# Performance work log

Measured on AMD Instinct MI355X. Metric: run time of the kernel, lower is better.

The kernel has to match this reference:

```python
import jax, jax.numpy as jnp
import numpy as np

B, T, C, H = 2, 2048, 2048, 16
HD = C // H  # 128 head dim
ROPE_BASE = 10000.0


def setup_inputs() -> dict:
    key = jax.random.key(0)
    k0, k1, k2 = jax.random.split(key, 3)
    x = jax.random.normal(k0, (B, T, C), dtype=jnp.float32)
    W_attn = jax.random.normal(k1, (C, 3 * C), dtype=jnp.float32) * 0.02
    b_attn = jnp.zeros((3 * C,), dtype=jnp.float32)
    W_proj = jax.random.normal(k2, (C, C), dtype=jnp.float32) * 0.02
    b_proj = jnp.zeros((C,), dtype=jnp.float32)
    # freqs_cis = exp(i * t * theta_j), represented as (cos, sin), shape [T, HD//2]
    inv_freq = 1.0 / (ROPE_BASE ** (jnp.arange(0, HD, 2, dtype=jnp.float32) / HD))
    freqs = jnp.outer(jnp.arange(T, dtype=jnp.float32), inv_freq)
    return {"x": x, "W_attn": W_attn, "b_attn": b_attn, "W_proj": W_proj,
            "b_proj": b_proj, "cos": jnp.cos(freqs), "sin": jnp.sin(freqs)}


def _apply_rope(v, cos, sin):
    # v: [B, T, H, HD]; pairs (v[..., 2i], v[..., 2i+1]) rotated by angle freqs[t, i]
    vr = v.reshape(v.shape[:-1] + (-1, 2))
    x0, x1 = vr[..., 0], vr[..., 1]
    c = cos[None, :, None, :]  # [1, T, 1, HD//2]
    s = sin[None, :, None, :]
    o0 = x0 * c - x1 * s
    o1 = x0 * s + x1 * c
    return jnp.stack([o0, o1], axis=-1).reshape(v.shape)


def reference(x, W_attn, b_attn, W_proj, b_proj, cos, sin):
    Bv, Tv, Cv = x.shape
    qkv = x @ W_attn + b_attn                      # [B, T, 3C]
    q, k, v = jnp.split(qkv, 3, axis=-1)
    q = q.reshape(Bv, Tv, H, HD)
    k = k.reshape(Bv, Tv, H, HD)
    v = v.reshape(Bv, Tv, H, HD)
    q = _apply_rope(q, cos, sin)
    k = _apply_rope(k, cos, sin)
    scale = 1.0 / jnp.sqrt(jnp.float32(HD))
    att = jnp.einsum('bqhd,bkhd->bhqk', q, k) * scale
    causal = jnp.tril(jnp.ones((Tv, Tv), dtype=bool))
    att = jnp.where(causal[None, None], att, jnp.finfo(att.dtype).min)
    att = jax.nn.softmax(att, axis=-1)
    y = jnp.einsum('bhqk,bkhd->bqhd', att, v).reshape(Bv, Tv, Cv)
    return y @ W_proj + b_proj
```

## Files before the change

### kernel.cpp

```cpp
#include <hip/hip_runtime.h>

typedef unsigned short u16;
typedef __attribute__((ext_vector_type(8))) short short8;
typedef __attribute__((ext_vector_type(4))) float f32x4;

#define TSEQ 2048
#define NHEAD 16
#define HDIM 128

__device__ __forceinline__ u16 f2bf(float x) {
    unsigned u = __float_as_uint(x);
    return (u16)((u + 0x7fffu + ((u >> 16) & 1u)) >> 16);
}
__device__ __forceinline__ float b2f(u16 h) {
    return __uint_as_float(((unsigned)h) << 16);
}
__device__ __forceinline__ void async16(const void* g, void* l) {
    __builtin_amdgcn_global_load_lds((__attribute__((address_space(1))) void*)(void*)g,
                                     (__attribute__((address_space(3))) void*)l, 16, 0, 0);
}
__device__ __forceinline__ f32x4 zero4() {
    f32x4 z = {0.f, 0.f, 0.f, 0.f};
    return z;
}

template <int CTRL>
__device__ __forceinline__ float dppf(float x) {
    return __int_as_float(__builtin_amdgcn_mov_dpp(__float_as_int(x), CTRL, 0xf, 0xf, true));
}
__device__ __forceinline__ float dpp_max16(float x) {
    x = fmaxf(x, dppf<0xB1>(x));
    x = fmaxf(x, dppf<0x4E>(x));
    x = fmaxf(x, dppf<0x141>(x));
    x = fmaxf(x, dppf<0x140>(x));
    return x;
}
__device__ __forceinline__ float dpp_sum16(float x) {
    x += dppf<0xB1>(x);
    x += dppf<0x4E>(x);
    x += dppf<0x141>(x);
    x += dppf<0x140>(x);
    return x;
}

__global__ void cast_bf16(const float4* __restrict__ in, ushort4* __restrict__ out, int n4) {
    int i = blockIdx.x * 256 + threadIdx.x;
    if (i < n4) {
        float4 v = in[i];
        ushort4 o;
        o.x = f2bf(v.x); o.y = f2bf(v.y); o.z = f2bf(v.z); o.w = f2bf(v.w);
        out[i] = o;
    }
}

__global__ void transpose_cast(const float* __restrict__ in, u16* __restrict__ out, int K, int N) {
    __shared__ float tile[64][65];
    int n0 = blockIdx.x * 64, k0 = blockIdx.y * 64;
    int tx = threadIdx.x & 63, ty = threadIdx.x >> 6;
#pragma unroll
    for (int i = 0; i < 16; i++) {
        int r = ty + i * 4;
        tile[r][tx] = in[(size_t)(k0 + r) * N + n0 + tx];
    }
    __syncthreads();
#pragma unroll
    for (int i = 0; i < 16; i++) {
        int r = ty + i * 4;
        out[(size_t)(n0 + r) * K + k0 + tx] = f2bf(tile[tx][r]);
    }
}

template <int MODE>
__global__ __launch_bounds__(256) void gemm_bt(
    const u16* __restrict__ A, const u16* __restrict__ Bt, const float* __restrict__ bias,
    float* __restrict__ outf, u16* __restrict__ qb, u16* __restrict__ kb, u16* __restrict__ vT,
    const float* __restrict__ cosp, const float* __restrict__ sinp,
    int M, int N, int K) {
    __shared__ __align__(16) u16 smem[8704];
    u16* As = smem;
    u16* Bs = smem + 4096;
    const int tid = threadIdx.x;
    const int wave = tid >> 6, lane = tid & 63;
    const int low = lane & 15, quad = lane >> 4;
    const int m0 = blockIdx.y * 128, n0 = blockIdx.x * 128;
    const int wm = (wave >> 1) * 64, wn = (wave & 1) * 64;
    const int ldr = lane >> 2;
    const int ldc = (lane & 3) * 8;

    f32x4 acc[4][4];
#pragma unroll
    for (int i = 0; i < 4; i++)
#pragma unroll
        for (int j = 0; j < 4; j++) acc[i][j] = zero4();

    for (int k0 = 0; k0 < K; k0 += 32) {
#pragma unroll
        for (int c = 0; c < 2; ++c) {
            const int chunk = wave * 2 + c;
            const int row = chunk * 16 + ldr;
            async16(A + (size_t)(m0 + row) * K + k0 + ldc, As + chunk * 512);
            async16(Bt + (size_t)(n0 + row) * K + k0 + ldc, Bs + chunk * 512);
        }
        __syncthreads();
        short8 af[4], bfv[4];
#pragma unroll
        for (int i = 0; i < 4; i++) af[i] = *(const short8*)(As + (wm + i * 16 + low) * 32 + quad * 8);
#pragma unroll
        for (int j = 0; j < 4; j++) bfv[j] = *(const short8*)(Bs + (wn + j * 16 + low) * 32 + quad * 8);
#pragma unroll
        for (int i = 0; i < 4; i++)
#pragma unroll
            for (int j = 0; j < 4; j++)
                acc[i][j] = __builtin_amdgcn_mfma_f32_16x16x32_bf16(af[i], bfv[j], acc[i][j], 0, 0, 0);
        __syncthreads();
    }

    if (MODE == 1) {
#pragma unroll
        for (int j = 0; j < 4; j++) {
            const int ng = n0 + wn + j * 16 + low;
            const float bv = bias[ng];
#pragma unroll
            for (int i = 0; i < 4; i++) {
                const int rbase = m0 + wm + i * 16 + quad * 4;
#pragma unroll
                for (int r = 0; r < 4; r++)
                    outf[(size_t)(rbase + r) * N + ng] = acc[i][j][r] + bv;
            }
        }
        return;
    }

    const int which = n0 >> 11;
    const int h = (n0 & 2047) >> 7;
    const int b = m0 >> 11, t0 = m0 & 2047;
    float bv[4];
#pragma unroll
    for (int j = 0; j < 4; j++) bv[j] = bias[n0 + wn + j * 16 + low];
    u16* epi = smem;

    if (which < 2) {
        u16* dst = (which == 0 ? qb : kb) + (((size_t)(b * NHEAD + h)) * TSEQ + t0) * HDIM;
#pragma unroll
        for (int pass = 0; pass < 2; pass++) {
            if ((wave >> 1) == pass) {
#pragma unroll
                for (int i = 0; i < 4; i++)
#pragma unroll
                    for (int j = 0; j < 4; j++)
#pragma unroll
                        for (int r = 0; r < 4; r++)
                            epi[(i * 16 + quad * 4 + r) * 136 + wn + j * 16 + low] =
                                f2bf(acc[i][j][r] + bv[j]);
            }
            __syncthreads();
            const int row = tid >> 2, dp = (tid & 3) * 32;
            const int t = t0 + pass * 64 + row;
            u16 vals[32];
#pragma unroll
            for (int q = 0; q < 4; q++)
                *(short8*)(vals + q * 8) = *(const short8*)(epi + row * 136 + dp + q * 8);
            float cs4[16], sn4[16];
#pragma unroll
            for (int q = 0; q < 4; q++) {
                *(float4*)(cs4 + q * 4) = *(const float4*)(cosp + (size_t)t * 64 + (dp >> 1) + q * 4);
                *(float4*)(sn4 + q * 4) = *(const float4*)(sinp + (size_t)t * 64 + (dp >> 1) + q * 4);
            }
            u16 outv[32];
#pragma unroll
            for (int p = 0; p < 16; p++) {
                float x0 = b2f(vals[2 * p]), x1 = b2f(vals[2 * p + 1]);
                outv[2 * p] = f2bf(x0 * cs4[p] - x1 * sn4[p]);
                outv[2 * p + 1] = f2bf(x0 * sn4[p] + x1 * cs4[p]);
            }
            u16* dr = dst + (size_t)(pass * 64 + row) * HDIM + dp;
#pragma unroll
            for (int q = 0; q < 4; q++)
                *(short8*)(dr + q * 8) = *(const short8*)(outv + q * 8);
            __syncthreads();
        }
    } else {
        u16* dst = vT + ((size_t)(b * NHEAD + h)) * HDIM * TSEQ + t0;
#pragma unroll
        for (int pass = 0; pass < 2; pass++) {
            if ((wave & 1) == pass) {
#pragma unroll
                for (int i = 0; i < 4; i++)
#pragma unroll
                    for (int j = 0; j < 4; j++)
#pragma unroll
                        for (int r = 0; r < 4; r++)
                            epi[(j * 16 + low) * 136 + wm + i * 16 + quad * 4 + r] =
                                f2bf(acc[i][j][r] + bv[j]);
            }
            __syncthreads();
            const int drow = tid >> 2, tc = (tid & 3) * 32;
            u16* dr = dst + (size_t)(pass * 64 + drow) * TSEQ + tc;
#pragma unroll
            for (int q = 0; q < 4; q++)
                *(short8*)(dr + q * 8) = *(const short8*)(epi + drow * 136 + tc + q * 8);
            __syncthreads();
        }
    }
}

__global__ __launch_bounds__(256) void flash_attn(const u16* __restrict__ qb, const u16* __restrict__ kb,
                                                  const u16* __restrict__ vT, u16* __restrict__ y) {
    __shared__ u16 Ks[64 * 128];
    __shared__ u16 Vs[128 * 64];
    __shared__ u16 Ps[4][16 * 72];
    const int tid = threadIdx.x;
    const int wave = tid >> 6, lane = tid & 63;
    const int low = lane & 15, quad = lane >> 4;
    const int bh = blockIdx.x;
    const int qt = 31 - blockIdx.y;
    const int q0 = qt * 64 + wave * 16;
    const float scale2 = 0.08838834764831845f * 1.44269504088896f;

    const u16* Qp = qb + ((size_t)bh * TSEQ + q0) * HDIM;
    short8 qf[4];
#pragma unroll
    for (int c = 0; c < 4; c++) qf[c] = *(const short8*)(Qp + (size_t)low * HDIM + c * 32 + quad * 8);

    f32x4 o[8];
#pragma unroll
    for (int d = 0; d < 8; d++) o[d] = zero4();
    float m_i[4], l_i[4];
#pragma unroll
    for (int r = 0; r < 4; r++) { m_i[r] = -1e30f; l_i[r] = 0.f; }

    const u16* Kb = kb + (size_t)bh * TSEQ * HDIM;
    const u16* Vb = vT + (size_t)bh * HDIM * TSEQ;
    u16* Pw = &Ps[wave][0];
    const int ntiles = qt + 1;

    const int krow = tid >> 4, kchunk = tid & 15;
    const int vrow = tid >> 3, vchunk = tid & 7;

    for (int kt = 0; kt < ntiles; ++kt) {
        const int kv0 = kt * 64;
#pragma unroll
        for (int j = 0; j < 4; j++) {
            const int row = j * 16 + krow;
            const int gc = kchunk ^ (row & 7);
            async16(Kb + (size_t)(kv0 + row) * HDIM + gc * 8, Ks + row * 128 + kchunk * 8);
        }
#pragma unroll
        for (int j = 0; j < 4; j++) {
            const int d = j * 32 + vrow;
            const int gc = vchunk ^ (d & 7);
            async16(Vb + (size_t)d * TSEQ + kv0 + gc * 8, Vs + d * 64 + vchunk * 8);
        }
        __syncthreads();

        f32x4 s[4];
#pragma unroll
        for (int h = 0; h < 4; h++) s[h] = zero4();
#pragma unroll
        for (int h = 0; h < 4; h++) {
            const int row = h * 16 + low;
#pragma unroll
            for (int c = 0; c < 4; c++) {
                const int cc = c * 4 + quad;
                short8 kf = *(const short8*)(Ks + row * 128 + (cc ^ (row & 7)) * 8);
                s[h] = __builtin_amdgcn_mfma_f32_16x16x32_bf16(qf[c], kf, s[h], 0, 0, 0);
            }
        }

        float alpha[4];
#pragma unroll
        for (int r = 0; r < 4; r++) {
            const int qg = q0 + quad * 4 + r;
            float sv[4];
#pragma unroll
            for (int h = 0; h < 4; h++)
                sv[h] = (kv0 + h * 16 + low <= qg) ? s[h][r] * scale2 : -1e30f;
            float mx = fmaxf(fmaxf(sv[0], sv[1]), fmaxf(sv[2], sv[3]));
            mx = dpp_max16(mx);
            float mnew = fmaxf(m_i[r], mx);
            alpha[r] = exp2f(m_i[r] - mnew);
            m_i[r] = mnew;
            float p0 = exp2f(sv[0] - mnew);
            float p1 = exp2f(sv[1] - mnew);
            float p2 = exp2f(sv[2] - mnew);
            float p3 = exp2f(sv[3] - mnew);
            float rs = (p0 + p1) + (p2 + p3);
            rs = dpp_sum16(rs);
            l_i[r] = l_i[r] * alpha[r] + rs;
            const int prow = (quad * 4 + r) * 72;
            Pw[prow + low] = f2bf(p0);
            Pw[prow + 16 + low] = f2bf(p1);
            Pw[prow + 32 + low] = f2bf(p2);
            Pw[prow + 48 + low] = f2bf(p3);
        }
        __threadfence_block();

#pragma unroll
        for (int d = 0; d < 8; ++d)
#pragma unroll
            for (int r = 0; r < 4; r++) o[d][r] *= alpha[r];

#pragma unroll
        for (int kc = 0; kc < 2; kc++) {
            short8 pf = *(const short8*)(Pw + low * 72 + kc * 32 + quad * 8);
#pragma unroll
            for (int dd = 0; dd < 8; ++dd) {
                const int vr = dd * 16 + low;
                const int cc = kc * 4 + quad;
                short8 vf = *(const short8*)(Vs + vr * 64 + (cc ^ (vr & 7)) * 8);
                o[dd] = __builtin_amdgcn_mfma_f32_16x16x32_bf16(pf, vf, o[dd], 0, 0, 0);
            }
        }
        __syncthreads();
    }

    const int b = bh >> 4, h = bh & 15;
#pragma unroll
    for (int r = 0; r < 4; r++) {
        float inv = 1.0f / l_i[r];
        size_t row = (size_t)(b * TSEQ + q0 + quad * 4 + r);
        u16* yp = y + row * 2048 + h * HDIM;
#pragma unroll
        for (int d = 0; d < 8; ++d) yp[d * 16 + low] = f2bf(o[d][r] * inv);
    }
}

extern "C" void kernel_launch(void* const* d_in, const int* in_sizes, int n_in,
                              void* d_out, int out_size, void* d_ws, size_t ws_size,
                              hipStream_t stream) {
    const float* x = (const float*)d_in[0];
    const float* Wa = (const float*)d_in[1];
    const float* ba = (const float*)d_in[2];
    const float* Wp = (const float*)d_in[3];
    const float* bp = (const float*)d_in[4];
    const float* cs = (const float*)d_in[5];
    const float* sn = (const float*)d_in[6];
    float* out = (float*)d_out;

    u16* xb = (u16*)d_ws;
    u16* Wab = xb + 8388608;
    u16* Wpb = Wab + 12582912;
    u16* qb = Wpb + 4194304;
    u16* kb = qb + 8388608;
    u16* vT = kb + 8388608;
    u16* y = xb;

    cast_bf16<<<8192, 256, 0, stream>>>((const float4*)x, (ushort4*)xb, 2097152);
    transpose_cast<<<dim3(96, 32), 256, 0, stream>>>(Wa, Wab, 2048, 6144);
    transpose_cast<<<dim3(32, 32), 256, 0, stream>>>(Wp, Wpb, 2048, 2048);
    gemm_bt<0><<<dim3(48, 32), 256, 0, stream>>>(xb, Wab, ba, nullptr, qb, kb, vT, cs, sn, 4096, 6144, 2048);
    flash_attn<<<dim3(32, 32), 256, 0, stream>>>(qb, kb, vT, y);
    gemm_bt<1><<<dim3(16, 32), 256, 0, stream>>>(y, Wpb, bp, out, nullptr, nullptr, nullptr, nullptr, nullptr, 4096, 2048, 2048);
}
```

Before: 455.6 us.

## Process two query tiles per attention block with double-buffered V prefetch

Each flash-attention block now handles 128 query rows as two 64-row halves that share every K/V tile loaded into LDS. This halves K/V global traffic and the number of blocks. The next K tile and a double-buffered V tile are prefetched asynchronously while softmax and PV run. Launch bounds hint occupancy for both kernels, and the RoPE epilogue is split into halves to reduce register pressure. The trade is doubled accumulator registers per wave and more per-block imbalance across the causal triangle.

```diff
diff --git a/kernel.cpp b/kernel.cpp
--- a/kernel.cpp
+++ b/kernel.cpp
@@ -71,7 +71,7 @@
 }
 
 template <int MODE>
-__global__ __launch_bounds__(256) void gemm_bt(
+__global__ __launch_bounds__(256, 5) void gemm_bt(
     const u16* __restrict__ A, const u16* __restrict__ Bt, const float* __restrict__ bias,
     float* __restrict__ outf, u16* __restrict__ qb, u16* __restrict__ kb, u16* __restrict__ vT,
     const float* __restrict__ cosp, const float* __restrict__ sinp,
@@ -154,29 +154,32 @@
                                 f2bf(acc[i][j][r] + bv[j]);
             }
             __syncthreads();
-            const int row = tid >> 2, dp = (tid & 3) * 32;
+            const int row = tid >> 2, dq = tid & 3;
             const int t = t0 + pass * 64 + row;
-            u16 vals[32];
-#pragma unroll
-            for (int q = 0; q < 4; q++)
-                *(short8*)(vals + q * 8) = *(const short8*)(epi + row * 136 + dp + q * 8);
-            float cs4[16], sn4[16];
-#pragma unroll
-            for (int q = 0; q < 4; q++) {
-                *(float4*)(cs4 + q * 4) = *(const float4*)(cosp + (size_t)t * 64 + (dp >> 1) + q * 4);
-                *(float4*)(sn4 + q * 4) = *(const float4*)(sinp + (size_t)t * 64 + (dp >> 1) + q * 4);
-            }
-            u16 outv[32];
-#pragma unroll
-            for (int p = 0; p < 16; p++) {
-                float x0 = b2f(vals[2 * p]), x1 = b2f(vals[2 * p + 1]);
-                outv[2 * p] = f2bf(x0 * cs4[p] - x1 * sn4[p]);
-                outv[2 * p + 1] = f2bf(x0 * sn4[p] + x1 * cs4[p]);
-            }
-            u16* dr = dst + (size_t)(pass * 64 + row) * HDIM + dp;
-#pragma unroll
-            for (int q = 0; q < 4; q++)
-                *(short8*)(dr + q * 8) = *(const short8*)(outv + q * 8);
+            const float* cb = cosp + (size_t)t * 64 + dq * 16;
+            const float* sb = sinp + (size_t)t * 64 + dq * 16;
+            const u16* er = epi + row * 136 + dq * 32;
+            u16* dr = dst + (size_t)(pass * 64 + row) * HDIM + dq * 32;
+#pragma unroll
+            for (int half = 0; half < 2; half++) {
+                u16 vals[16];
+                *(short8*)(vals) = *(const short8*)(er + half * 16);
+                *(short8*)(vals + 8) = *(const short8*)(er + half * 16 + 8);
+                float cs[8], sn[8];
+                *(float4*)(cs) = *(const float4*)(cb + half * 8);
+                *(float4*)(cs + 4) = *(const float4*)(cb + half * 8 + 4);
+                *(float4*)(sn) = *(const float4*)(sb + half * 8);
+                *(float4*)(sn + 4) = *(const float4*)(sb + half * 8 + 4);
+                u16 ov[16];
+#pragma unroll
+                for (int p = 0; p < 8; p++) {
+                    float x0 = b2f(vals[2 * p]), x1 = b2f(vals[2 * p + 1]);
+                    ov[2 * p] = f2bf(x0 * cs[p] - x1 * sn[p]);
+                    ov[2 * p + 1] = f2bf(x0 * sn[p] + x1 * cs[p]);
+                }
+                *(short8*)(dr + half * 16) = *(const short8*)(ov);
+                *(short8*)(dr + half * 16 + 8) = *(const short8*)(ov + 8);
+            }
             __syncthreads();
         }
     } else {
@@ -204,124 +207,200 @@
     }
 }
 
-__global__ __launch_bounds__(256) void flash_attn(const u16* __restrict__ qb, const u16* __restrict__ kb,
-                                                  const u16* __restrict__ vT, u16* __restrict__ y) {
+__global__ __launch_bounds__(256, 2) void flash_attn(const u16* __restrict__ qg, const u16* __restrict__ kg,
+                                                     const u16* __restrict__ vT, u16* __restrict__ y) {
     __shared__ u16 Ks[64 * 128];
-    __shared__ u16 Vs[128 * 64];
+    __shared__ u16 Vs[2][128 * 64];
     __shared__ u16 Ps[4][16 * 72];
     const int tid = threadIdx.x;
     const int wave = tid >> 6, lane = tid & 63;
     const int low = lane & 15, quad = lane >> 4;
-    const int bh = blockIdx.x;
-    const int qt = 31 - blockIdx.y;
-    const int q0 = qt * 64 + wave * 16;
+    const int qt = 15 - blockIdx.x;
+    const int bh = blockIdx.y;
+    const int qa = qt * 128 + wave * 16;
+    const int qbr = qa + 64;
     const float scale2 = 0.08838834764831845f * 1.44269504088896f;
 
-    const u16* Qp = qb + ((size_t)bh * TSEQ + q0) * HDIM;
-    short8 qf[4];
-#pragma unroll
-    for (int c = 0; c < 4; c++) qf[c] = *(const short8*)(Qp + (size_t)low * HDIM + c * 32 + quad * 8);
-
-    f32x4 o[8];
-#pragma unroll
-    for (int d = 0; d < 8; d++) o[d] = zero4();
-    float m_i[4], l_i[4];
-#pragma unroll
-    for (int r = 0; r < 4; r++) { m_i[r] = -1e30f; l_i[r] = 0.f; }
-
-    const u16* Kb = kb + (size_t)bh * TSEQ * HDIM;
+    const u16* Qp = qg + (size_t)bh * TSEQ * HDIM;
+    short8 qfA[4], qfB[4];
+#pragma unroll
+    for (int c = 0; c < 4; c++) {
+        qfA[c] = *(const short8*)(Qp + (size_t)(qa + low) * HDIM + c * 32 + quad * 8);
+        qfB[c] = *(const short8*)(Qp + (size_t)(qbr + low) * HDIM + c * 32 + quad * 8);
+    }
+
+    f32x4 oA[8], oB[8];
+#pragma unroll
+    for (int d = 0; d < 8; d++) { oA[d] = zero4(); oB[d] = zero4(); }
+    float mA[4], lA[4], mB[4], lB[4];
+#pragma unroll
+    for (int r = 0; r < 4; r++) { mA[r] = -1e30f; lA[r] = 0.f; mB[r] = -1e30f; lB[r] = 0.f; }
+
+    const u16* Kb = kg + (size_t)bh * TSEQ * HDIM;
     const u16* Vb = vT + (size_t)bh * HDIM * TSEQ;
     u16* Pw = &Ps[wave][0];
-    const int ntiles = qt + 1;
+    const int ntiles = 2 * qt + 2;
 
     const int krow = tid >> 4, kchunk = tid & 15;
     const int vrow = tid >> 3, vchunk = tid & 7;
 
+#pragma unroll
+    for (int j = 0; j < 4; j++) {
+        const int row = j * 16 + krow;
+        async16(Kb + (size_t)row * HDIM + (kchunk ^ (row & 7)) * 8, Ks + row * 128 + kchunk * 8);
+    }
+#pragma unroll
+    for (int j = 0; j < 4; j++) {
+        const int d = j * 32 + vrow;
+        async16(Vb + (size_t)d * TSEQ + (vchunk ^ (d & 7)) * 8, Vs[0] + d * 64 + vchunk * 8);
+    }
+
     for (int kt = 0; kt < ntiles; ++kt) {
         const int kv0 = kt * 64;
-#pragma unroll
-        for (int j = 0; j < 4; j++) {
-            const int row = j * 16 + krow;
-            const int gc = kchunk ^ (row & 7);
-            async16(Kb + (size_t)(kv0 + row) * HDIM + gc * 8, Ks + row * 128 + kchunk * 8);
-        }
-#pragma unroll
-        for (int j = 0; j < 4; j++) {
-            const int d = j * 32 + vrow;
-            const int gc = vchunk ^ (d & 7);
-            async16(Vb + (size_t)d * TSEQ + kv0 + gc * 8, Vs + d * 64 + vchunk * 8);
-        }
+        const int cur = kt & 1;
         __syncthreads();
 
-        f32x4 s[4];
-#pragma unroll
-        for (int h = 0; h < 4; h++) s[h] = zero4();
+        const bool activeA = (kv0 <= qa + 15);
+        f32x4 sA[4], sB[4];
+#pragma unroll
+        for (int h = 0; h < 4; h++) { sA[h] = zero4(); sB[h] = zero4(); }
+        if (activeA) {
+#pragma unroll
+            for (int h = 0; h < 4; h++) {
+                const int row = h * 16 + low;
+#pragma unroll
+                for (int c = 0; c < 4; c++) {
+                    short8 kf = *(const short8*)(Ks + row * 128 + (((c * 4 + quad) ^ (row & 7))) * 8);
+                    sA[h] = __builtin_amdgcn_mfma_f32_16x16x32_bf16(qfA[c], kf, sA[h], 0, 0, 0);
+                }
+            }
+        }
 #pragma unroll
         for (int h = 0; h < 4; h++) {
             const int row = h * 16 + low;
 #pragma unroll
             for (int c = 0; c < 4; c++) {
-                const int cc = c * 4 + quad;
-                short8 kf = *(const short8*)(Ks + row * 128 + (cc ^ (row & 7)) * 8);
-                s[h] = __builtin_amdgcn_mfma_f32_16x16x32_bf16(qf[c], kf, s[h], 0, 0, 0);
-            }
-        }
-
-        float alpha[4];
-#pragma unroll
-        for (int r = 0; r < 4; r++) {
-            const int qg = q0 + quad * 4 + r;
-            float sv[4];
-#pragma unroll
-            for (int h = 0; h < 4; h++)
-                sv[h] = (kv0 + h * 16 + low <= qg) ? s[h][r] * scale2 : -1e30f;
-            float mx = fmaxf(fmaxf(sv[0], sv[1]), fmaxf(sv[2], sv[3]));
-            mx = dpp_max16(mx);
-            float mnew = fmaxf(m_i[r], mx);
-            alpha[r] = exp2f(m_i[r] - mnew);
-            m_i[r] = mnew;
-            float p0 = exp2f(sv[0] - mnew);
-            float p1 = exp2f(sv[1] - mnew);
-            float p2 = exp2f(sv[2] - mnew);
-            float p3 = exp2f(sv[3] - mnew);
-            float rs = (p0 + p1) + (p2 + p3);
-            rs = dpp_sum16(rs);
-            l_i[r] = l_i[r] * alpha[r] + rs;
-            const int prow = (quad * 4 + r) * 72;
-            Pw[prow + low] = f2bf(p0);
-            Pw[prow + 16 + low] = f2bf(p1);
-            Pw[prow + 32 + low] = f2bf(p2);
-            Pw[prow + 48 + low] = f2bf(p3);
-        }
-        __threadfence_block();
-
-#pragma unroll
-        for (int d = 0; d < 8; ++d)
-#pragma unroll
-            for (int r = 0; r < 4; r++) o[d][r] *= alpha[r];
-
-#pragma unroll
-        for (int kc = 0; kc < 2; kc++) {
-            short8 pf = *(const short8*)(Pw + low * 72 + kc * 32 + quad * 8);
-#pragma unroll
-            for (int dd = 0; dd < 8; ++dd) {
-                const int vr = dd * 16 + low;
-                const int cc = kc * 4 + quad;
-                short8 vf = *(const short8*)(Vs + vr * 64 + (cc ^ (vr & 7)) * 8);
-                o[dd] = __builtin_amdgcn_mfma_f32_16x16x32_bf16(pf, vf, o[dd], 0, 0, 0);
+                short8 kf = *(const short8*)(Ks + row * 128 + (((c * 4 + quad) ^ (row & 7))) * 8);
+                sB[h] = __builtin_amdgcn_mfma_f32_16x16x32_bf16(qfB[c], kf, sB[h], 0, 0, 0);
             }
         }
         __syncthreads();
+
+        if (kt + 1 < ntiles) {
+            const int nkv = kv0 + 64;
+#pragma unroll
+            for (int j = 0; j < 4; j++) {
+                const int row = j * 16 + krow;
+                async16(Kb + (size_t)(nkv + row) * HDIM + (kchunk ^ (row & 7)) * 8,
+                        Ks + row * 128 + kchunk * 8);
+            }
+            u16* vdst = Vs[cur ^ 1];
+#pragma unroll
+            for (int j = 0; j < 4; j++) {
+                const int d = j * 32 + vrow;
+                async16(Vb + (size_t)d * TSEQ + nkv + (vchunk ^ (d & 7)) * 8, vdst + d * 64 + vchunk * 8);
+            }
+        }
+
+        const u16* Vcur = Vs[cur];
+        if (activeA) {
+            float alpha[4];
+#pragma unroll
+            for (int r = 0; r < 4; r++) {
+                const int qrow = qa + quad * 4 + r;
+                float sv[4];
+#pragma unroll
+                for (int h = 0; h < 4; h++)
+                    sv[h] = (kv0 + h * 16 + low <= qrow) ? sA[h][r] * scale2 : -1e30f;
+                float mx = fmaxf(fmaxf(sv[0], sv[1]), fmaxf(sv[2], sv[3]));
+                mx = dpp_max16(mx);
+                float mnew = fmaxf(mA[r], mx);
+                alpha[r] = exp2f(mA[r] - mnew);
+                mA[r] = mnew;
+                float p0 = exp2f(sv[0] - mnew), p1 = exp2f(sv[1] - mnew);
+                float p2 = exp2f(sv[2] - mnew), p3 = exp2f(sv[3] - mnew);
+                float rs = (p0 + p1) + (p2 + p3);
+                rs = dpp_sum16(rs);
+                lA[r] = lA[r] * alpha[r] + rs;
+                const int prow = (quad * 4 + r) * 72;
+                Pw[prow + low] = f2bf(p0);
+                Pw[prow + 16 + low] = f2bf(p1);
+                Pw[prow + 32 + low] = f2bf(p2);
+                Pw[prow + 48 + low] = f2bf(p3);
+            }
+            __threadfence_block();
+#pragma unroll
+            for (int d = 0; d < 8; ++d)
+#pragma unroll
+                for (int r = 0; r < 4; r++) oA[d][r] *= alpha[r];
+#pragma unroll
+            for (int kc = 0; kc < 2; kc++) {
+                short8 pf = *(const short8*)(Pw + low * 72 + kc * 32 + quad * 8);
+#pragma unroll
+                for (int dd = 0; dd < 8; ++dd) {
+                    const int vr = dd * 16 + low;
+                    short8 vf = *(const short8*)(Vcur + vr * 64 + (((kc * 4 + quad) ^ (vr & 7))) * 8);
+                    oA[dd] = __builtin_amdgcn_mfma_f32_16x16x32_bf16(pf, vf, oA[dd], 0, 0, 0);
+                }
+            }
+        }
+        {
+            float alpha[4];
+#pragma unroll
+            for (int r = 0; r < 4; r++) {
+                const int qrow = qbr + quad * 4 + r;
+                float sv[4];
+#pragma unroll
+                for (int h = 0; h < 4; h++)
+                    sv[h] = (kv0 + h * 16 + low <= qrow) ? sB[h][r] * scale2 : -1e30f;
+                float mx = fmaxf(fmaxf(sv[0], sv[1]), fmaxf(sv[2], sv[3]));
+                mx = dpp_max16(mx);
+                float mnew = fmaxf(mB[r], mx);
+                alpha[r] = exp2f(mB[r] - mnew);
+                mB[r] = mnew;
+                float p0 = exp2f(sv[0] - mnew), p1 = exp2f(sv[1] - mnew);
+                float p2 = exp2f(sv[2] - mnew), p3 = exp2f(sv[3] - mnew);
+                float rs = (p0 + p1) + (p2 + p3);
+                rs = dpp_sum16(rs);
+                lB[r] = lB[r] * alpha[r] + rs;
+                const int prow = (quad * 4 + r) * 72;
+                Pw[prow + low] = f2bf(p0);
+                Pw[prow + 16 + low] = f2bf(p1);
+                Pw[prow + 32 + low] = f2bf(p2);
+                Pw[prow + 48 + low] = f2bf(p3);
+            }
+            __threadfence_block();
+#pragma unroll
+            for (int d = 0; d < 8; ++d)
+#pragma unroll
+                for (int r = 0; r < 4; r++) oB[d][r] *= alpha[r];
+#pragma unroll
+            for (int kc = 0; kc < 2; kc++) {
+                short8 pf = *(const short8*)(Pw + low * 72 + kc * 32 + quad * 8);
+#pragma unroll
+                for (int dd = 0; dd < 8; ++dd) {
+                    const int vr = dd * 16 + low;
+                    short8 vf = *(const short8*)(Vcur + vr * 64 + (((kc * 4 + quad) ^ (vr & 7))) * 8);
+                    oB[dd] = __builtin_amdgcn_mfma_f32_16x16x32_bf16(pf, vf, oB[dd], 0, 0, 0);
+                }
+            }
+        }
     }
 
     const int b = bh >> 4, h = bh & 15;
 #pragma unroll
     for (int r = 0; r < 4; r++) {
-        float inv = 1.0f / l_i[r];
-        size_t row = (size_t)(b * TSEQ + q0 + quad * 4 + r);
-        u16* yp = y + row * 2048 + h * HDIM;
-#pragma unroll
-        for (int d = 0; d < 8; ++d) yp[d * 16 + low] = f2bf(o[d][r] * inv);
+        float invA = 1.0f / lA[r];
+        float invB = 1.0f / lB[r];
+        size_t rowA = (size_t)(b * TSEQ + qa + quad * 4 + r);
+        size_t rowB = (size_t)(b * TSEQ + qbr + quad * 4 + r);
+        u16* ypA = y + rowA * 2048 + h * HDIM;
+        u16* ypB = y + rowB * 2048 + h * HDIM;
+#pragma unroll
+        for (int d = 0; d < 8; ++d) {
+            ypA[d * 16 + low] = f2bf(oA[d][r] * invA);
+            ypB[d * 16 + low] = f2bf(oB[d][r] * invB);
+        }
     }
 }
 
@@ -349,6 +428,6 @@
     transpose_cast<<<dim3(96, 32), 256, 0, stream>>>(Wa, Wab, 2048, 6144);
     transpose_cast<<<dim3(32, 32), 256, 0, stream>>>(Wp, Wpb, 2048, 2048);
     gemm_bt<0><<<dim3(48, 32), 256, 0, stream>>>(xb, Wab, ba, nullptr, qb, kb, vT, cs, sn, 4096, 6144, 2048);
-    flash_attn<<<dim3(32, 32), 256, 0, stream>>>(qb, kb, vT, y);
+    flash_attn<<<dim3(16, 32), 256, 0, stream>>>(qb, kb, vT, y);
     gemm_bt<1><<<dim3(16, 32), 256, 0, stream>>>(y, Wpb, bp, out, nullptr, nullptr, nullptr, nullptr, nullptr, 4096, 2048, 2048);
 }
```

New measurement: 508.6 us. 1.12x slower.
